# Performance work log

Measured on AMD Instinct MI355X. Metric: run time of the kernel, lower is better.

## Reference

```python
import jax, jax.numpy as jnp
import numpy as np

BBOX_XFORM_CLIP = float(np.log(1000.0 / 16.0))
WX, WY, WW, WH = 10.0, 10.0, 5.0, 5.0  # torchvision default box-coder weights


def setup_inputs() -> dict:
    key = jax.random.key(0)
    B, P, C, E = 8, 25000, 81, 256
    H, W = 800, 800
    k1, k2, k3, k4, k5 = jax.random.split(key, 5)
    N = B * P
    class_logits = jax.random.normal(k1, (N, C), dtype=jnp.float32)
    box_regression = jax.random.normal(k2, (N, C * 4), dtype=jnp.float32) * 0.1
    id_embedding = jax.random.normal(k3, (N, E), dtype=jnp.float32)
    # valid proposals: x1<x2, y1<y2, inside the image
    xy = jax.random.uniform(k4, (B, P, 2), dtype=jnp.float32) * (W - 65.0)
    wh = jax.random.uniform(k5, (B, P, 2), dtype=jnp.float32) * 63.0 + 1.0
    proposals = jnp.concatenate([xy, xy + wh], axis=-1)  # [B,P,4] x1,y1,x2,y2
    return {
        'class_logits': class_logits,
        'box_regression': box_regression,
        'id_embedding': id_embedding,
        'proposals': proposals,
        'img_h': H,
        'img_w': W,
    }


def _decode_boxes(box_regression, proposals_flat):
    # torchvision BoxCoder.decode, vectorized. proposals_flat: [N,4]
    N = proposals_flat.shape[0]
    C = box_regression.shape[1] // 4
    deltas = box_regression.reshape(N, C, 4)
    x1, y1, x2, y2 = jnp.split(proposals_flat, 4, axis=-1)  # each [N,1]
    w = x2 - x1
    h = y2 - y1
    cx = x1 + 0.5 * w
    cy = y1 + 0.5 * h
    dx = deltas[..., 0] / WX  # [N,C]
    dy = deltas[..., 1] / WY
    dw = jnp.minimum(deltas[..., 2] / WW, BBOX_XFORM_CLIP)
    dh = jnp.minimum(deltas[..., 3] / WH, BBOX_XFORM_CLIP)
    pcx = dx * w + cx
    pcy = dy * h + cy
    pw = jnp.exp(dw) * w
    ph = jnp.exp(dh) * h
    boxes = jnp.stack(
        [pcx - 0.5 * pw, pcy - 0.5 * ph, pcx + 0.5 * pw, pcy + 0.5 * ph], axis=-1
    )  # [N,C,4]
    return boxes


def reference(class_logits, box_regression, id_embedding, proposals, img_h, img_w):
    B, P, _ = proposals.shape
    C = class_logits.shape[-1]
    Hf = jnp.float32(img_h)
    Wf = jnp.float32(img_w)

    boxes = _decode_boxes(box_regression, proposals.reshape(B * P, 4))  # [N,C,4]
    # clip_boxes_to_image
    bx = jnp.clip(boxes[..., 0::2], 0.0, Wf)
    by = jnp.clip(boxes[..., 1::2], 0.0, Hf)
    boxes = jnp.stack([bx[..., 0], by[..., 0], bx[..., 1], by[..., 1]], axis=-1)

    scores = jax.nn.softmax(class_logits, axis=-1)  # [N,C]

    # per-image split (uniform counts -> reshape), drop background class 0
    boxes = boxes.reshape(B, P, C, 4)[:, :, 1:, :]          # [B,P,C-1,4]
    scores = scores.reshape(B, P, C)[:, :, 1:]              # [B,P,C-1]
    id_embs = id_embedding.reshape(B, P, -1)                # [B,P,E]
    labels = jnp.broadcast_to(jnp.arange(1, C, dtype=jnp.int32), (B, P, C - 1))
    roi_idxs = jnp.broadcast_to(
        jnp.arange(P, dtype=jnp.int32)[None, :, None], (B, P, C - 1)
    )
    return boxes, scores, id_embs, labels, roi_idxs
```

## Files before the change

### kernel.cpp

```cpp
#include <hip/hip_runtime.h>

#define N_TOT   200000
#define C_CLS   81
#define P_PER   25000
#define CM1     80


typedef float f4 __attribute__((ext_vector_type(4)));

#define DEC_BLOCKS 62500u
#define SM_BLOCKS  50000u
#define CP_BLOCKS  25000u
#define LR_BLOCKS  15625u
#define CP_HALF    6400000u

__global__ __launch_bounds__(256) void fused_kernel(
    const float* __restrict__ logits,
    const f4*    __restrict__ box_reg4,
    const f4*    __restrict__ id_emb4,
    const f4*    __restrict__ proposals4,
    const int*   __restrict__ img_h_p,
    const int*   __restrict__ img_w_p,
    float* __restrict__ out)
{
    f4*    out_boxes   = (f4*)out;
    float* out_scores  = out + 64000000u;
    f4*    out_ids     = (f4*)(out + 80000000u);
    f4*    out_labels4 = (f4*)(out + 131200000u);
    f4*    out_roi4    = (f4*)(out + 147200000u);

    unsigned int b = blockIdx.x;

    if (b < DEC_BLOCKS) {
        unsigned int tid  = b * 256u + threadIdx.x;
        unsigned int n    = tid / CM1;
        unsigned int cidx = tid - n * CM1;
        unsigned int c    = cidx + 1u;

        const float Wf = (float)img_w_p[0];
        const float Hf = (float)img_h_p[0];

        const f4 pr = proposals4[n];
        float w  = pr.z - pr.x;
        float h  = pr.w - pr.y;
        float cx = pr.x + 0.5f * w;
        float cy = pr.y + 0.5f * h;

        const f4 d = __builtin_nontemporal_load(&box_reg4[(size_t)n * C_CLS + c]);

        const float CLIP = 4.135166556742356f;
        float dx = d.x * 0.1f;
        float dy = d.y * 0.1f;
        float dw = fminf(d.z * 0.2f, CLIP);
        float dh = fminf(d.w * 0.2f, CLIP);

        float pcx = dx * w + cx;
        float pcy = dy * h + cy;
        float pw  = expf(dw) * w;
        float ph  = expf(dh) * h;

        float x1 = fminf(fmaxf(pcx - 0.5f * pw, 0.0f), Wf);
        float y1 = fminf(fmaxf(pcy - 0.5f * ph, 0.0f), Hf);
        float x2 = fminf(fmaxf(pcx + 0.5f * pw, 0.0f), Wf);
        float y2 = fminf(fmaxf(pcy + 0.5f * ph, 0.0f), Hf);

        f4 bx; bx.x = x1; bx.y = y1; bx.z = x2; bx.w = y2;
        __builtin_nontemporal_store(bx, &out_boxes[tid]);
    } else if (b < DEC_BLOCKS + SM_BLOCKS) {
        unsigned int wave = (b - DEC_BLOCKS) * 4u + (threadIdx.x >> 6);
        unsigned int lane = threadIdx.x & 63u;

        const float* row = logits + (size_t)wave * C_CLS;
        float v0 = __builtin_nontemporal_load(&row[lane]);
        float v1 = (lane < 17u) ? __builtin_nontemporal_load(&row[64u + lane]) : -INFINITY;

        float m = fmaxf(v0, v1);
        #pragma unroll
        for (int off = 32; off; off >>= 1) m = fmaxf(m, __shfl_xor(m, off, 64));

        float e0 = expf(v0 - m);
        float e1 = (lane < 17u) ? expf(v1 - m) : 0.0f;

        float s = e0 + e1;
        #pragma unroll
        for (int off = 32; off; off >>= 1) s += __shfl_xor(s, off, 64);

        float inv = 1.0f / s;
        float* o = out_scores + (size_t)wave * CM1;
        if (lane >= 1u) __builtin_nontemporal_store(e0 * inv, &o[lane - 1u]);
        if (lane < 17u) __builtin_nontemporal_store(e1 * inv, &o[63u + lane]);
    } else if (b < DEC_BLOCKS + SM_BLOCKS + CP_BLOCKS) {
        unsigned int i = (b - DEC_BLOCKS - SM_BLOCKS) * 256u + threadIdx.x;
        f4 a0 = __builtin_nontemporal_load(&id_emb4[i]);
        f4 a1 = __builtin_nontemporal_load(&id_emb4[i + CP_HALF]);
        __builtin_nontemporal_store(a0, &out_ids[i]);
        __builtin_nontemporal_store(a1, &out_ids[i + CP_HALF]);
    } else {
        unsigned int j = (b - DEC_BLOCKS - SM_BLOCKS - CP_BLOCKS) * 256u + threadIdx.x;
        unsigned int n  = j / 20u;
        unsigned int cb = (j - n * 20u) * 4u;
        f4 lv; lv.x = (float)(cb + 1u); lv.y = (float)(cb + 2u);
               lv.z = (float)(cb + 3u); lv.w = (float)(cb + 4u);
        float r = (float)(n % P_PER);
        f4 rv; rv.x = r; rv.y = r; rv.z = r; rv.w = r;
        __builtin_nontemporal_store(lv, &out_labels4[j]);
        __builtin_nontemporal_store(rv, &out_roi4[j]);
    }
}

extern "C" void kernel_launch(void* const* d_in, const int* in_sizes, int n_in,
                              void* d_out, int out_size, void* d_ws, size_t ws_size,
                              hipStream_t stream) {
    const float* class_logits = (const float*)d_in[0];
    const float* box_reg      = (const float*)d_in[1];
    const float* id_emb       = (const float*)d_in[2];
    const float* proposals    = (const float*)d_in[3];
    const int*   img_h        = (const int*)d_in[4];
    const int*   img_w        = (const int*)d_in[5];

    dim3 grid(DEC_BLOCKS + SM_BLOCKS + CP_BLOCKS + LR_BLOCKS), block(256);
    fused_kernel<<<grid, block, 0, stream>>>(
        class_logits, (const f4*)box_reg, (const f4*)id_emb, (const f4*)proposals,
        img_h, img_w, (float*)d_out);
}
```

Baseline: 219.1 us.

## Coarsen decode and copy work per thread, stage softmax through LDS for vector stores

The box-decode branch now has each thread handle four consecutive classes of one proposal, so the proposal load and its derived values are reused and the decode block count drops by four. The embedding copy has each thread move four float4 chunks instead of two, halving those blocks. Softmax results are written to shared memory and then stored as 20 float4 per row instead of scalar stores. This cuts block count and index arithmetic at the cost of more registers, fewer threads in flight for the memory-bound branches, and an added __syncthreads in the softmax branch.

Result: slower. 504.1 us (+130.1%).

```diff
diff --git a/kernel.cpp b/kernel.cpp
--- a/kernel.cpp
+++ b/kernel.cpp
@@ -8,11 +8,14 @@
 
 typedef float f4 __attribute__((ext_vector_type(4)));
 
-#define DEC_BLOCKS 62500u
+#define DEC_BLOCKS 15625u
 #define SM_BLOCKS  50000u
-#define CP_BLOCKS  25000u
+#define CP_BLOCKS  12500u
 #define LR_BLOCKS  15625u
-#define CP_HALF    6400000u
+#define SM_BASE    (DEC_BLOCKS)
+#define CP_BASE    (DEC_BLOCKS + SM_BLOCKS)
+#define LR_BASE    (DEC_BLOCKS + SM_BLOCKS + CP_BLOCKS)
+#define CP_QTR     3200000u
 
 __global__ __launch_bounds__(256) void fused_kernel(
     const float* __restrict__ logits,
@@ -23,8 +26,10 @@
     const int*   __restrict__ img_w_p,
     float* __restrict__ out)
 {
+    __shared__ float sbuf[4][80];
+
     f4*    out_boxes   = (f4*)out;
-    float* out_scores  = out + 64000000u;
+    f4*    out_scores4 = (f4*)(out + 64000000u);
     f4*    out_ids     = (f4*)(out + 80000000u);
     f4*    out_labels4 = (f4*)(out + 131200000u);
     f4*    out_roi4    = (f4*)(out + 147200000u);
@@ -32,10 +37,9 @@
     unsigned int b = blockIdx.x;
 
     if (b < DEC_BLOCKS) {
-        unsigned int tid  = b * 256u + threadIdx.x;
-        unsigned int n    = tid / CM1;
-        unsigned int cidx = tid - n * CM1;
-        unsigned int c    = cidx + 1u;
+        unsigned int j  = b * 256u + threadIdx.x;
+        unsigned int n  = j / 20u;
+        unsigned int cb = (j - n * 20u) * 4u;
 
         const float Wf = (float)img_w_p[0];
         const float Hf = (float)img_h_p[0];
@@ -46,33 +50,38 @@
         float cx = pr.x + 0.5f * w;
         float cy = pr.y + 0.5f * h;
 
-        const f4 d = __builtin_nontemporal_load(&box_reg4[(size_t)n * C_CLS + c]);
+        const size_t rbase = (size_t)n * C_CLS + cb + 1u;
+        const size_t obase = (size_t)n * CM1 + cb;
+        const float CLIP = 4.135166556742356f;
 
-        const float CLIP = 4.135166556742356f;
-        float dx = d.x * 0.1f;
-        float dy = d.y * 0.1f;
-        float dw = fminf(d.z * 0.2f, CLIP);
-        float dh = fminf(d.w * 0.2f, CLIP);
+        #pragma unroll
+        for (unsigned int k = 0; k < 4; ++k) {
+            const f4 d = __builtin_nontemporal_load(&box_reg4[rbase + k]);
+            float dx = d.x * 0.1f;
+            float dy = d.y * 0.1f;
+            float dw = fminf(d.z * 0.2f, CLIP);
+            float dh = fminf(d.w * 0.2f, CLIP);
 
-        float pcx = dx * w + cx;
-        float pcy = dy * h + cy;
-        float pw  = expf(dw) * w;
-        float ph  = expf(dh) * h;
+            float pcx = dx * w + cx;
+            float pcy = dy * h + cy;
+            float pw  = expf(dw) * w;
+            float ph  = expf(dh) * h;
 
-        float x1 = fminf(fmaxf(pcx - 0.5f * pw, 0.0f), Wf);
-        float y1 = fminf(fmaxf(pcy - 0.5f * ph, 0.0f), Hf);
-        float x2 = fminf(fmaxf(pcx + 0.5f * pw, 0.0f), Wf);
-        float y2 = fminf(fmaxf(pcy + 0.5f * ph, 0.0f), Hf);
-
-        f4 bx; bx.x = x1; bx.y = y1; bx.z = x2; bx.w = y2;
-        __builtin_nontemporal_store(bx, &out_boxes[tid]);
-    } else if (b < DEC_BLOCKS + SM_BLOCKS) {
-        unsigned int wave = (b - DEC_BLOCKS) * 4u + (threadIdx.x >> 6);
+            f4 bx;
+            bx.x = fminf(fmaxf(pcx - 0.5f * pw, 0.0f), Wf);
+            bx.y = fminf(fmaxf(pcy - 0.5f * ph, 0.0f), Hf);
+            bx.z = fminf(fmaxf(pcx + 0.5f * pw, 0.0f), Wf);
+            bx.w = fminf(fmaxf(pcy + 0.5f * ph, 0.0f), Hf);
+            __builtin_nontemporal_store(bx, &out_boxes[obase + k]);
+        }
+    } else if (b < CP_BASE) {
+        unsigned int wrel = threadIdx.x >> 6;
+        unsigned int row  = (b - SM_BASE) * 4u + wrel;
         unsigned int lane = threadIdx.x & 63u;
 
-        const float* row = logits + (size_t)wave * C_CLS;
-        float v0 = __builtin_nontemporal_load(&row[lane]);
-        float v1 = (lane < 17u) ? __builtin_nontemporal_load(&row[64u + lane]) : -INFINITY;
+        const float* rp = logits + (size_t)row * C_CLS;
+        float v0 = __builtin_nontemporal_load(&rp[lane]);
+        float v1 = (lane < 17u) ? __builtin_nontemporal_load(&rp[64u + lane]) : -INFINITY;
 
         float m = fmaxf(v0, v1);
         #pragma unroll
@@ -86,17 +95,23 @@
         for (int off = 32; off; off >>= 1) s += __shfl_xor(s, off, 64);
 
         float inv = 1.0f / s;
-        float* o = out_scores + (size_t)wave * CM1;
-        if (lane >= 1u) __builtin_nontemporal_store(e0 * inv, &o[lane - 1u]);
-        if (lane < 17u) __builtin_nontemporal_store(e1 * inv, &o[63u + lane]);
-    } else if (b < DEC_BLOCKS + SM_BLOCKS + CP_BLOCKS) {
-        unsigned int i = (b - DEC_BLOCKS - SM_BLOCKS) * 256u + threadIdx.x;
-        f4 a0 = __builtin_nontemporal_load(&id_emb4[i]);
-        f4 a1 = __builtin_nontemporal_load(&id_emb4[i + CP_HALF]);
-        __builtin_nontemporal_store(a0, &out_ids[i]);
-        __builtin_nontemporal_store(a1, &out_ids[i + CP_HALF]);
+        float* srow = sbuf[wrel];
+        if (lane >= 1u) srow[lane - 1u] = e0 * inv;
+        if (lane < 17u) srow[63u + lane] = e1 * inv;
+        __syncthreads();
+        if (lane < 20u) {
+            f4 v = ((const f4*)srow)[lane];
+            __builtin_nontemporal_store(v, &out_scores4[(size_t)row * 20u + lane]);
+        }
+    } else if (b < LR_BASE) {
+        unsigned int i = (b - CP_BASE) * 256u + threadIdx.x;
+        #pragma unroll
+        for (unsigned int k = 0; k < 4; ++k) {
+            f4 a = __builtin_nontemporal_load(&id_emb4[i + k * CP_QTR]);
+            __builtin_nontemporal_store(a, &out_ids[i + k * CP_QTR]);
+        }
     } else {
-        unsigned int j = (b - DEC_BLOCKS - SM_BLOCKS - CP_BLOCKS) * 256u + threadIdx.x;
+        unsigned int j = (b - LR_BASE) * 256u + threadIdx.x;
         unsigned int n  = j / 20u;
         unsigned int cb = (j - n * 20u) * 4u;
         f4 lv; lv.x = (float)(cb + 1u); lv.y = (float)(cb + 2u);
```
